# Optimization experiments

Measured on AMD Instinct MI355X. Metric: run time of the kernel, lower is better.

The kernel has to match this reference:

```python
import jax, jax.numpy as jnp
import numpy as np

D_MODEL = 768
STATE_N = 16
BATCH = 8
SEQ = 2048


def setup_inputs() -> dict:
    key = jax.random.key(0)
    ks = jax.random.split(key, 12)
    d, n = D_MODEL, STATE_N
    s = 0.02
    inp = {
        "x": jax.random.normal(ks[0], (BATCH, SEQ, d), dtype=jnp.float32),
        # A_log init as in module: log(arange(1..N)) repeated over d_model
        "A_log": jnp.log(jnp.tile(jnp.arange(1, n + 1, dtype=jnp.float32)[None, :], (d, 1))),
        "D_param": jnp.ones((d,), dtype=jnp.float32),
        "B_proj_w": jax.random.normal(ks[1], (n, d), dtype=jnp.float32) * s,
        "C_proj_w": jax.random.normal(ks[2], (n, d), dtype=jnp.float32) * s,
        "delta_w": jax.random.normal(ks[3], (d, d), dtype=jnp.float32) * s,
        "delta_b": jax.random.normal(ks[4], (d,), dtype=jnp.float32) * s,
        "in_w": jax.random.normal(ks[5], (2 * d, d), dtype=jnp.float32) * s,
        "in_b": jax.random.normal(ks[6], (2 * d,), dtype=jnp.float32) * s,
        "out_w": jax.random.normal(ks[7], (d, d), dtype=jnp.float32) * s,
        "out_b": jax.random.normal(ks[8], (d,), dtype=jnp.float32) * s,
        "conv_w": jax.random.normal(ks[9], (d, 1, 3), dtype=jnp.float32) * s,  # depthwise [D,1,K]
        "conv_b": jax.random.normal(ks[10], (d,), dtype=jnp.float32) * s,
    }
    return inp


def _forward(x, A_log, D_param, B_proj_w, C_proj_w, delta_w, delta_b,
             in_w, in_b, out_w, out_b, conv_w, conv_b):
    A = -jnp.exp(A_log)  # [D, N]
    xz = jnp.einsum("bld,ed->ble", x, in_w) + in_b  # [B, L, 2D]
    x_in, z = jnp.split(xz, 2, axis=-1)
    # depthwise conv1d, padding=1, groups=D (cross-correlation, same as torch)
    x_c = jax.lax.conv_general_dilated(
        jnp.transpose(x_in, (0, 2, 1)), conv_w,
        window_strides=(1,), padding=((1, 1),),
        feature_group_count=x.shape[-1],
        dimension_numbers=("NCH", "OIH", "NCH"))
    x_conv = jnp.transpose(x_c, (0, 2, 1)) + conv_b  # [B, L, D]
    x_conv = jax.nn.silu(x_conv)
    delta = jax.nn.softplus(jnp.einsum("bld,ed->ble", x_conv, delta_w) + delta_b)  # [B,L,D]
    B_sel = jnp.einsum("bld,nd->bln", x_conv, B_proj_w)  # [B, L, N]
    C_sel = jnp.einsum("bld,nd->bln", x_conv, C_proj_w)  # [B, L, N]

    Bsz, L, D = x.shape
    N = A.shape[1]

    def step(h, t_in):
        dt, b_t, c_t, x_t = t_in  # [B,D], [B,N], [B,N], [B,D]
        A_bar = jnp.exp(dt[:, :, None] * A[None, :, :])           # [B,D,N]
        h = A_bar * h + (dt[:, :, None] * b_t[:, None, :]) * x_t[:, :, None]
        y_t = jnp.sum(h * c_t[:, None, :], axis=-1)               # [B,D]
        return h, y_t

    xs = (jnp.transpose(delta, (1, 0, 2)), jnp.transpose(B_sel, (1, 0, 2)),
          jnp.transpose(C_sel, (1, 0, 2)), jnp.transpose(x_conv, (1, 0, 2)))
    h0 = jnp.zeros((Bsz, D, N), dtype=x.dtype)
    _, ys = jax.lax.scan(step, h0, xs)
    y = jnp.transpose(ys, (1, 0, 2))  # [B, L, D]

    y = y + x_conv * D_param[None, None, :]
    y = y * jax.nn.silu(z)
    return jnp.einsum("bld,ed->ble", y, out_w) + out_b


def reference(x, A_log, D_param, B_proj_w, C_proj_w, delta_w, delta_b,
              in_w, in_b, out_w, out_b, conv_w, conv_b):
    return _forward(x, A_log, D_param, B_proj_w, C_proj_w, delta_w, delta_b,
                    in_w, in_b, out_w, out_b, conv_w, conv_b)
```

## Files before the change

### kernel.cpp

```cpp
#include <hip/hip_runtime.h>
#include <hip/hip_bf16.h>

#define D_MODEL 768
#define SEQL    2048
#define BATCH   8
#define NSTATE  16
#define NCHUNK  32
#define TCHUNK  64

typedef __attribute__((ext_vector_type(8))) short short8;
typedef __attribute__((ext_vector_type(4))) float f32x4;

typedef const __attribute__((address_space(1))) unsigned int gas1_t;
typedef __attribute__((address_space(3))) unsigned int las3_t;

__device__ __forceinline__ void gload_lds16(const void* g, void* l) {
  __builtin_amdgcn_global_load_lds((gas1_t*)g, (las3_t*)l, 16, 0, 0);
}

__device__ __forceinline__ float b2f(short s) {
  return __uint_as_float(((unsigned)(unsigned short)s) << 16);
}
__device__ __forceinline__ short f2b(float f) {
  __hip_bfloat16 h = __float2bfloat16(f);
  return *reinterpret_cast<short*>(&h);
}

__global__ __launch_bounds__(256) void prep_all(
    const float* __restrict__ x, const float* __restrict__ in_w,
    const float* __restrict__ delta_w, const float* __restrict__ Bp,
    const float* __restrict__ Cp, const float* __restrict__ out_w,
    const float* __restrict__ A_log,
    __hip_bfloat16* __restrict__ xb, __hip_bfloat16* __restrict__ w_in,
    __hip_bfloat16* __restrict__ w_dbc, __hip_bfloat16* __restrict__ w_out,
    float* __restrict__ A2) {
  int i = blockIdx.x * 256 + threadIdx.x;
  if (i < 3145728) {
    int j = i * 4;
    float4 v = *(const float4*)(x + j);
    xb[j + 0] = __float2bfloat16(v.x);
    xb[j + 1] = __float2bfloat16(v.y);
    xb[j + 2] = __float2bfloat16(v.z);
    xb[j + 3] = __float2bfloat16(v.w);
    return;
  }
  i -= 3145728;
  if (i < 1536 * 768) { w_in[i] = __float2bfloat16(in_w[i]); return; }
  i -= 1536 * 768;
  if (i < 896 * 768) {
    int row = i / 768, col = i - row * 768;
    float v;
    if (row < 768)      v = delta_w[row * 768 + col];
    else if (row < 784) v = Bp[(row - 768) * 768 + col];
    else if (row < 800) v = Cp[(row - 784) * 768 + col];
    else                v = 0.f;
    w_dbc[i] = __float2bfloat16(v);
    return;
  }
  i -= 896 * 768;
  if (i < 768 * 768) { w_out[i] = __float2bfloat16(out_w[i]); return; }
  i -= 768 * 768;
  A2[i] = -expf(A_log[i]) * 1.44269504088896f;
}

template <int MODE>
__global__ __launch_bounds__(256, 3) void gemm128tb(
    const __hip_bfloat16* __restrict__ Amat, const __hip_bfloat16* __restrict__ Bw,
    const float* __restrict__ bias, void* __restrict__ out0,
    void* __restrict__ out1, void* __restrict__ out2, const int gxn) {
  constexpr int K  = 768;
  constexpr int KT = 24;
  __shared__ char lds[49152];
  const int tid  = threadIdx.x;
  const int lane = tid & 63, wave = tid >> 6;
  const int wr = wave >> 1, wc = wave & 1;

  const int nwg = gridDim.x, id = blockIdx.x;
  const int swz = (id & 7) * (nwg >> 3) + (id >> 3);
  const int tm = swz / gxn, tn = swz - tm * gxn;
  const int rowA0 = tm * 128, rowB0 = tn * 128;

  const int srow = tid >> 2;
  const int scol = (((tid & 3) ^ ((srow >> 1) & 3)) << 3);
  const __hip_bfloat16* gA = Amat + (size_t)(rowA0 + srow) * K + scol;
  const __hip_bfloat16* gB = Bw   + (size_t)(rowB0 + srow) * K + scol;
  const int ldst = tid << 4;

  const int frow = lane & 15, fq = lane >> 4;
  const int pc = (fq << 4) ^ (((frow >> 1) & 3) << 4);
  const int aoff = ((wr * 64 + frow) << 6) + pc;
  const int boff = ((wc * 64 + frow) << 6) + pc;

  f32x4 acc[4][4];
#pragma unroll
  for (int m = 0; m < 4; ++m)
#pragma unroll
    for (int n = 0; n < 4; ++n) acc[m][n] = (f32x4){0.f, 0.f, 0.f, 0.f};

#define STAGE(buf, kt)                                                          \
  {                                                                             \
    const __hip_bfloat16* sA = gA + (kt) * 32;                                  \
    const __hip_bfloat16* sB = gB + (kt) * 32;                                  \
    char* dA = lds + (buf) * 16384 + ldst;                                      \
    char* dB = dA + 8192;                                                       \
    gload_lds16(sA, dA);                                                        \
    gload_lds16(sA + (size_t)64 * K, dA + 4096);                                \
    gload_lds16(sB, dB);                                                        \
    gload_lds16(sB + (size_t)64 * K, dB + 4096);                                \
  }
#define VMW(n) asm volatile("s_waitcnt vmcnt(" #n ")" ::: "memory")
#define BAR    __builtin_amdgcn_s_barrier()

  STAGE(0, 0);
  STAGE(1, 1);
  VMW(4);
  BAR;

  int bc = 0;
  for (int kt = 0; kt < KT; ++kt) {
    short8 a[4], b[4];
    const char* ba = lds + bc * 16384;
#pragma unroll
    for (int m = 0; m < 4; ++m) a[m] = *(const short8*)(ba + aoff + m * 1024);
#pragma unroll
    for (int n = 0; n < 4; ++n) b[n] = *(const short8*)(ba + 8192 + boff + n * 1024);
    const bool st = (kt + 2 < KT);
    if (st) {
      const int b2 = bc + 2 >= 3 ? bc - 1 : bc + 2;
      STAGE(b2, kt + 2);
    }
    __builtin_amdgcn_s_setprio(1);
#pragma unroll
    for (int m = 0; m < 4; ++m)
#pragma unroll
      for (int n = 0; n < 4; ++n)
        acc[m][n] = __builtin_amdgcn_mfma_f32_16x16x32_bf16(a[m], b[n], acc[m][n], 0, 0, 0);
    __builtin_amdgcn_s_setprio(0);
    if (st)                VMW(4);
    else if (kt + 2 == KT) VMW(0);
    BAR;
    bc = bc + 1 >= 3 ? 0 : bc + 1;
  }

#pragma unroll
  for (int m = 0; m < 4; ++m) {
    const int grow0 = rowA0 + wr * 64 + m * 16 + fq * 4;
#pragma unroll
    for (int n = 0; n < 4; ++n) {
      const int gcol = rowB0 + wc * 64 + n * 16 + frow;
#pragma unroll
      for (int i = 0; i < 4; ++i) {
        const size_t grow = grow0 + i;
        float v = acc[m][n][i];
        if (MODE == 0) {
          v += bias[gcol];
          if (gcol < 768)
            ((__hip_bfloat16*)out0)[grow * 768 + gcol] = __float2bfloat16(v);
          else
            ((__hip_bfloat16*)out1)[grow * 768 + gcol - 768] = __float2bfloat16(v);
        } else if (MODE == 1) {
          if (gcol < 768) {
            v += bias[gcol];
            float sp = (v > 20.f) ? v : log1pf(expf(v));
            ((__hip_bfloat16*)out0)[grow * 768 + gcol] = __float2bfloat16(sp);
          } else if (gcol < 784) {
            ((float*)out1)[grow * 16 + (gcol - 768)] = v;
          } else if (gcol < 800) {
            ((float*)out2)[grow * 16 + (gcol - 784)] = v;
          }
        } else {
          ((float*)out0)[grow * 768 + gcol] = v + bias[gcol];
        }
      }
    }
  }
#undef STAGE
#undef VMW
#undef BAR
}

__global__ __launch_bounds__(256) void conv_silu8(
    const __hip_bfloat16* __restrict__ xin, const float* __restrict__ conv_w,
    const float* __restrict__ conv_b, __hip_bfloat16* __restrict__ xc) {
  const int idx = blockIdx.x * 256 + threadIdx.x;
  const int d8 = (idx % 96) * 8;
  const int t  = (idx / 96) % SEQL;
  const size_t base = (size_t)idx * 8;

  short8 x0 = *(const short8*)(xin + base);
  short8 xm = {}, xp = {};
  if (t > 0)        xm = *(const short8*)(xin + base - 768);
  if (t < SEQL - 1) xp = *(const short8*)(xin + base + 768);

  const float4* cw4 = (const float4*)(conv_w + d8 * 3);
  float4 cw[6];
#pragma unroll
  for (int q = 0; q < 6; ++q) cw[q] = cw4[q];
  float4 cb0 = *(const float4*)(conv_b + d8);
  float4 cb1 = *(const float4*)(conv_b + d8 + 4);
  const float* cwf = (const float*)cw;
  const float* cbf0 = (const float*)&cb0;
  const float* cbf1 = (const float*)&cb1;

  short8 r;
#pragma unroll
  for (int e = 0; e < 8; ++e) {
    float acc = (e < 4) ? cbf0[e] : cbf1[e - 4];
    acc = fmaf(cwf[e * 3 + 0], b2f(xm[e]), acc);
    acc = fmaf(cwf[e * 3 + 1], b2f(x0[e]), acc);
    acc = fmaf(cwf[e * 3 + 2], b2f(xp[e]), acc);
    const float sig = 1.f / (1.f + __expf(-acc));
    r[e] = f2b(acc * sig);
  }
  *(short8*)(xc + base) = r;
}

__global__ __launch_bounds__(256) void scan_pass1(
    const __hip_bfloat16* __restrict__ delta, const __hip_bfloat16* __restrict__ xconv,
    const float* __restrict__ Bsel, const float* __restrict__ A2,
    float* __restrict__ sumdt, float* __restrict__ Sbuf) {
  const int d = blockIdx.x * 256 + threadIdx.x;
  const int b = blockIdx.y, c = blockIdx.z;
  __shared__ float sB[TCHUNK * 16];
  ((float4*)sB)[threadIdx.x] =
      ((const float4*)(Bsel + ((size_t)b * SEQL + c * TCHUNK) * 16))[threadIdx.x];
  __syncthreads();

  float a2[16];
#pragma unroll
  for (int n = 0; n < 16; ++n) a2[n] = A2[d * 16 + n];
  float h[16] = {};
  float sdt = 0.f;
  const size_t base = ((size_t)b * SEQL + c * TCHUNK) * 768 + d;
  for (int t = 0; t < TCHUNK; ++t) {
    const float dt = b2f(((const short*)delta)[base + (size_t)t * 768]);
    const float x = b2f(((const short*)xconv)[base + (size_t)t * 768]);
    sdt += dt;
    const float dtx = dt * x;
    const float* Br = &sB[t * 16];
#pragma unroll
    for (int n = 0; n < 16; ++n) {
      const float a = exp2f(dt * a2[n]);
      h[n] = fmaf(a, h[n], dtx * Br[n]);
    }
  }
  sumdt[((size_t)b * NCHUNK + c) * 768 + d] = sdt;
#pragma unroll
  for (int n = 0; n < 16; ++n)
    Sbuf[(((size_t)b * NCHUNK + c) * 16 + n) * 768 + d] = h[n];
}

__global__ __launch_bounds__(256) void scan_carry(
    const float* __restrict__ sumdt, const float* __restrict__ Sbuf,
    const float* __restrict__ A2, float* __restrict__ Hin) {
  const int idx = blockIdx.x * 256 + threadIdx.x;
  const int d = idx % 768;
  const int n = (idx / 768) & 15;
  const int b = idx / (768 * 16);
  const float a2 = A2[d * 16 + n];
  float h = 0.f;
  for (int c = 0; c < NCHUNK; ++c) {
    const size_t hb = (((size_t)(b * NCHUNK + c)) * 16 + n) * 768 + d;
    Hin[hb] = h;
    const float sd = sumdt[(b * NCHUNK + c) * 768 + d];
    h = fmaf(exp2f(sd * a2), h, Sbuf[hb]);
  }
}

__global__ __launch_bounds__(256) void scan_pass3(
    const __hip_bfloat16* __restrict__ delta, const __hip_bfloat16* __restrict__ xconv,
    const __hip_bfloat16* __restrict__ zb, const float* __restrict__ Bsel,
    const float* __restrict__ Csel, const float* __restrict__ A2,
    const float* __restrict__ Hin, const float* __restrict__ Dp,
    __hip_bfloat16* __restrict__ yg) {
  const int d = blockIdx.x * 256 + threadIdx.x;
  const int b = blockIdx.y, c = blockIdx.z;
  __shared__ float sB[TCHUNK * 16], sC[TCHUNK * 16];
  {
    const size_t off = ((size_t)b * SEQL + c * TCHUNK) * 16;
    ((float4*)sB)[threadIdx.x] = ((const float4*)(Bsel + off))[threadIdx.x];
    ((float4*)sC)[threadIdx.x] = ((const float4*)(Csel + off))[threadIdx.x];
  }
  __syncthreads();

  float a2[16];
#pragma unroll
  for (int n = 0; n < 16; ++n) a2[n] = A2[d * 16 + n];
  float h[16];
  {
    const size_t hb = ((size_t)b * NCHUNK + c) * 16 * 768 + d;
#pragma unroll
    for (int n = 0; n < 16; ++n) h[n] = Hin[hb + (size_t)n * 768];
  }
  const float Dpd = Dp[d];
  const size_t base = ((size_t)b * SEQL + c * TCHUNK) * 768 + d;
  for (int t = 0; t < TCHUNK; ++t) {
    const float dt = b2f(((const short*)delta)[base + (size_t)t * 768]);
    const float x = b2f(((const short*)xconv)[base + (size_t)t * 768]);
    const float dtx = dt * x;
    const float* Br = &sB[t * 16];
    const float* Cr = &sC[t * 16];
    float y = 0.f;
#pragma unroll
    for (int n = 0; n < 16; ++n) {
      const float a = exp2f(dt * a2[n]);
      h[n] = fmaf(a, h[n], dtx * Br[n]);
      y = fmaf(h[n], Cr[n], y);
    }
    const float z = b2f(((const short*)zb)[base + (size_t)t * 768]);
    const float sig = 1.f / (1.f + __expf(-z));
    const float out = (y + x * Dpd) * (z * sig);
    yg[base + (size_t)t * 768] = __float2bfloat16(out);
  }
}

extern "C" void kernel_launch(void* const* d_in, const int* in_sizes, int n_in,
                              void* d_out, int out_size, void* d_ws, size_t ws_size,
                              hipStream_t stream) {
  const float* x       = (const float*)d_in[0];
  const float* A_log   = (const float*)d_in[1];
  const float* D_param = (const float*)d_in[2];
  const float* B_proj  = (const float*)d_in[3];
  const float* C_proj  = (const float*)d_in[4];
  const float* delta_w = (const float*)d_in[5];
  const float* delta_b = (const float*)d_in[6];
  const float* in_w    = (const float*)d_in[7];
  const float* in_b    = (const float*)d_in[8];
  const float* out_w   = (const float*)d_in[9];
  const float* out_b   = (const float*)d_in[10];
  const float* conv_w  = (const float*)d_in[11];
  const float* conv_b  = (const float*)d_in[12];

  char* ws = (char*)d_ws;
  __hip_bfloat16* xb       = (__hip_bfloat16*)(ws + 0);
  __hip_bfloat16* w_in_b   = (__hip_bfloat16*)(ws + 25165824);
  __hip_bfloat16* w_dbc_b  = (__hip_bfloat16*)(ws + 27525120);
  __hip_bfloat16* w_out_b  = (__hip_bfloat16*)(ws + 28901376);
  float*          A2       = (float*)(ws + 30081024);
  __hip_bfloat16* xin_b    = (__hip_bfloat16*)(ws + 30130176);
  __hip_bfloat16* z_b      = (__hip_bfloat16*)(ws + 55296000);
  __hip_bfloat16* xconv_b  = (__hip_bfloat16*)(ws + 80461824);
  __hip_bfloat16* delta_bf = (__hip_bfloat16*)(ws + 105627648);
  float*          Bsel     = (float*)(ws + 130793472);
  float*          Csel     = (float*)(ws + 131842048);
  float*          sumdt    = (float*)(ws + 132890624);
  float*          Sbuf     = (float*)(ws + 133677056);
  float*          Hin      = (float*)(ws + 146259968);
  __hip_bfloat16* yg       = xb;

  const int BLD = BATCH * SEQL * D_MODEL;

  prep_all<<<21936, 256, 0, stream>>>(x, in_w, delta_w, B_proj, C_proj, out_w, A_log,
                                      xb, w_in_b, w_dbc_b, w_out_b, A2);
  gemm128tb<0><<<1536, 256, 0, stream>>>(xb, w_in_b, in_b, xin_b, z_b, nullptr, 12);
  conv_silu8<<<BLD / 8 / 256, 256, 0, stream>>>(xin_b, conv_w, conv_b, xconv_b);
  gemm128tb<1><<<896, 256, 0, stream>>>(xconv_b, w_dbc_b, delta_b, delta_bf, Bsel, Csel, 7);
  scan_pass1<<<dim3(3, BATCH, NCHUNK), 256, 0, stream>>>(delta_bf, xconv_b, Bsel, A2, sumdt, Sbuf);
  scan_carry<<<384, 256, 0, stream>>>(sumdt, Sbuf, A2, Hin);
  scan_pass3<<<dim3(3, BATCH, NCHUNK), 256, 0, stream>>>(delta_bf, xconv_b, z_b, Bsel, Csel, A2,
                                                         Hin, D_param, yg);
  gemm128tb<2><<<768, 256, 0, stream>>>(yg, w_out_b, out_b, (float*)d_out, nullptr, nullptr, 6);
}
```

Baseline: 347.0 us.

## Store bf16 activations and weights in pre-tiled swizzled layout for contiguous GEMM staging

All bf16 intermediates (x, weights, xin, z, xconv, delta, y) are now written in a 128x32 tile-major layout with the LDS swizzle already applied. The GEMM stages each 8KB k-tile as one contiguous block instead of strided row segments. prep_all also converts 8 elements per thread with packed 16-byte stores. The cost is scattered 2-byte stores in GEMM epilogues and scan kernels whose per-timestep accesses now land in different cache lines. The changed access pattern in the scans could hurt coalescing.

```diff
diff --git a/kernel.cpp b/kernel.cpp
--- a/kernel.cpp
+++ b/kernel.cpp
@@ -26,49 +26,80 @@
   return *reinterpret_cast<short*>(&h);
 }
 
+__device__ __forceinline__ unsigned tix(int r, int k) {
+  return (unsigned)((((r >> 7) * 24 + (k >> 5)) << 13) + ((r & 127) << 6) +
+                    ((((k >> 3) ^ ((r >> 1) & 3)) & 3) << 4) + ((k & 7) << 1));
+}
+
+__device__ __forceinline__ short8 pack8(const float* v) {
+  short8 o;
+#pragma unroll
+  for (int e = 0; e < 8; ++e) o[e] = f2b(v[e]);
+  return o;
+}
+
 __global__ __launch_bounds__(256) void prep_all(
     const float* __restrict__ x, const float* __restrict__ in_w,
     const float* __restrict__ delta_w, const float* __restrict__ Bp,
     const float* __restrict__ Cp, const float* __restrict__ out_w,
     const float* __restrict__ A_log,
-    __hip_bfloat16* __restrict__ xb, __hip_bfloat16* __restrict__ w_in,
-    __hip_bfloat16* __restrict__ w_dbc, __hip_bfloat16* __restrict__ w_out,
+    char* __restrict__ xb, char* __restrict__ w_in,
+    char* __restrict__ w_dbc, char* __restrict__ w_out,
     float* __restrict__ A2) {
   int i = blockIdx.x * 256 + threadIdx.x;
-  if (i < 3145728) {
-    int j = i * 4;
-    float4 v = *(const float4*)(x + j);
-    xb[j + 0] = __float2bfloat16(v.x);
-    xb[j + 1] = __float2bfloat16(v.y);
-    xb[j + 2] = __float2bfloat16(v.z);
-    xb[j + 3] = __float2bfloat16(v.w);
+  if (i < 16384 * 96) {
+    const int r = i / 96, k8 = i - r * 96;
+    float v[8];
+    *(float4*)(v) = *(const float4*)(x + (size_t)r * 768 + k8 * 8);
+    *(float4*)(v + 4) = *(const float4*)(x + (size_t)r * 768 + k8 * 8 + 4);
+    *(short8*)(xb + tix(r, k8 * 8)) = pack8(v);
     return;
   }
-  i -= 3145728;
-  if (i < 1536 * 768) { w_in[i] = __float2bfloat16(in_w[i]); return; }
-  i -= 1536 * 768;
-  if (i < 896 * 768) {
-    int row = i / 768, col = i - row * 768;
-    float v;
-    if (row < 768)      v = delta_w[row * 768 + col];
-    else if (row < 784) v = Bp[(row - 768) * 768 + col];
-    else if (row < 800) v = Cp[(row - 784) * 768 + col];
-    else                v = 0.f;
-    w_dbc[i] = __float2bfloat16(v);
+  i -= 16384 * 96;
+  if (i < 1536 * 96) {
+    const int r = i / 96, k8 = i - r * 96;
+    float v[8];
+    *(float4*)(v) = *(const float4*)(in_w + (size_t)r * 768 + k8 * 8);
+    *(float4*)(v + 4) = *(const float4*)(in_w + (size_t)r * 768 + k8 * 8 + 4);
+    *(short8*)(w_in + tix(r, k8 * 8)) = pack8(v);
     return;
   }
-  i -= 896 * 768;
-  if (i < 768 * 768) { w_out[i] = __float2bfloat16(out_w[i]); return; }
-  i -= 768 * 768;
+  i -= 1536 * 96;
+  if (i < 896 * 96) {
+    const int r = i / 96, k8 = i - r * 96;
+    float v[8];
+    const float* src = (r < 768)   ? delta_w + (size_t)r * 768
+                       : (r < 784) ? Bp + (size_t)(r - 768) * 768
+                       : (r < 800) ? Cp + (size_t)(r - 784) * 768
+                                   : nullptr;
+    if (src) {
+      *(float4*)(v) = *(const float4*)(src + k8 * 8);
+      *(float4*)(v + 4) = *(const float4*)(src + k8 * 8 + 4);
+    } else {
+#pragma unroll
+      for (int e = 0; e < 8; ++e) v[e] = 0.f;
+    }
+    *(short8*)(w_dbc + tix(r, k8 * 8)) = pack8(v);
+    return;
+  }
+  i -= 896 * 96;
+  if (i < 768 * 96) {
+    const int r = i / 96, k8 = i - r * 96;
+    float v[8];
+    *(float4*)(v) = *(const float4*)(out_w + (size_t)r * 768 + k8 * 8);
+    *(float4*)(v + 4) = *(const float4*)(out_w + (size_t)r * 768 + k8 * 8 + 4);
+    *(short8*)(w_out + tix(r, k8 * 8)) = pack8(v);
+    return;
+  }
+  i -= 768 * 96;
   A2[i] = -expf(A_log[i]) * 1.44269504088896f;
 }
 
 template <int MODE>
 __global__ __launch_bounds__(256, 3) void gemm128tb(
-    const __hip_bfloat16* __restrict__ Amat, const __hip_bfloat16* __restrict__ Bw,
+    const char* __restrict__ Amat, const char* __restrict__ Bw,
     const float* __restrict__ bias, void* __restrict__ out0,
     void* __restrict__ out1, void* __restrict__ out2, const int gxn) {
-  constexpr int K  = 768;
   constexpr int KT = 24;
   __shared__ char lds[49152];
   const int tid  = threadIdx.x;
@@ -78,12 +109,9 @@
   const int nwg = gridDim.x, id = blockIdx.x;
   const int swz = (id & 7) * (nwg >> 3) + (id >> 3);
   const int tm = swz / gxn, tn = swz - tm * gxn;
-  const int rowA0 = tm * 128, rowB0 = tn * 128;
-
-  const int srow = tid >> 2;
-  const int scol = (((tid & 3) ^ ((srow >> 1) & 3)) << 3);
-  const __hip_bfloat16* gA = Amat + (size_t)(rowA0 + srow) * K + scol;
-  const __hip_bfloat16* gB = Bw   + (size_t)(rowB0 + srow) * K + scol;
+
+  const char* gA = Amat + ((size_t)tm * KT) * 8192 + (tid << 4);
+  const char* gB = Bw   + ((size_t)tn * KT) * 8192 + (tid << 4);
   const int ldst = tid << 4;
 
   const int frow = lane & 15, fq = lane >> 4;
@@ -99,14 +127,14 @@
 
 #define STAGE(buf, kt)                                                          \
   {                                                                             \
-    const __hip_bfloat16* sA = gA + (kt) * 32;                                  \
-    const __hip_bfloat16* sB = gB + (kt) * 32;                                  \
+    const char* sA = gA + (kt) * 8192;                                          \
+    const char* sB = gB + (kt) * 8192;                                          \
     char* dA = lds + (buf) * 16384 + ldst;                                      \
     char* dB = dA + 8192;                                                       \
     gload_lds16(sA, dA);                                                        \
-    gload_lds16(sA + (size_t)64 * K, dA + 4096);                                \
+    gload_lds16(sA + 4096, dA + 4096);                                          \
     gload_lds16(sB, dB);                                                        \
-    gload_lds16(sB + (size_t)64 * K, dB + 4096);                                \
+    gload_lds16(sB + 4096, dB + 4096);                                          \
   }
 #define VMW(n) asm volatile("s_waitcnt vmcnt(" #n ")" ::: "memory")
 #define BAR    __builtin_amdgcn_s_barrier()
@@ -142,6 +170,7 @@
     bc = bc + 1 >= 3 ? 0 : bc + 1;
   }
 
+  const int rowA0 = tm * 128, rowB0 = tn * 128;
 #pragma unroll
   for (int m = 0; m < 4; ++m) {
     const int grow0 = rowA0 + wr * 64 + m * 16 + fq * 4;
@@ -150,26 +179,26 @@
       const int gcol = rowB0 + wc * 64 + n * 16 + frow;
 #pragma unroll
       for (int i = 0; i < 4; ++i) {
-        const size_t grow = grow0 + i;
+        const int grow = grow0 + i;
         float v = acc[m][n][i];
         if (MODE == 0) {
           v += bias[gcol];
           if (gcol < 768)
-            ((__hip_bfloat16*)out0)[grow * 768 + gcol] = __float2bfloat16(v);
+            *(short*)((char*)out0 + tix(grow, gcol)) = f2b(v);
           else
-            ((__hip_bfloat16*)out1)[grow * 768 + gcol - 768] = __float2bfloat16(v);
+            *(short*)((char*)out1 + tix(grow, gcol - 768)) = f2b(v);
         } else if (MODE == 1) {
           if (gcol < 768) {
             v += bias[gcol];
             float sp = (v > 20.f) ? v : log1pf(expf(v));
-            ((__hip_bfloat16*)out0)[grow * 768 + gcol] = __float2bfloat16(sp);
+            *(short*)((char*)out0 + tix(grow, gcol)) = f2b(sp);
           } else if (gcol < 784) {
-            ((float*)out1)[grow * 16 + (gcol - 768)] = v;
+            ((float*)out1)[(size_t)grow * 16 + (gcol - 768)] = v;
           } else if (gcol < 800) {
-            ((float*)out2)[grow * 16 + (gcol - 784)] = v;
+            ((float*)out2)[(size_t)grow * 16 + (gcol - 784)] = v;
           }
         } else {
-          ((float*)out0)[grow * 768 + gcol] = v + bias[gcol];
+          ((float*)out0)[(size_t)grow * 768 + gcol] = v + bias[gcol];
         }
       }
     }
@@ -180,17 +209,17 @@
 }
 
 __global__ __launch_bounds__(256) void conv_silu8(
-    const __hip_bfloat16* __restrict__ xin, const float* __restrict__ conv_w,
-    const float* __restrict__ conv_b, __hip_bfloat16* __restrict__ xc) {
+    const char* __restrict__ xin, const float* __restrict__ conv_w,
+    const float* __restrict__ conv_b, char* __restrict__ xc) {
   const int idx = blockIdx.x * 256 + threadIdx.x;
-  const int d8 = (idx % 96) * 8;
-  const int t  = (idx / 96) % SEQL;
-  const size_t base = (size_t)idx * 8;
-
-  short8 x0 = *(const short8*)(xin + base);
+  const int r  = idx / 96;
+  const int d8 = (idx - r * 96) * 8;
+  const int t  = r & (SEQL - 1);
+
+  short8 x0 = *(const short8*)(xin + tix(r, d8));
   short8 xm = {}, xp = {};
-  if (t > 0)        xm = *(const short8*)(xin + base - 768);
-  if (t < SEQL - 1) xp = *(const short8*)(xin + base + 768);
+  if (t > 0)        xm = *(const short8*)(xin + tix(r - 1, d8));
+  if (t < SEQL - 1) xp = *(const short8*)(xin + tix(r + 1, d8));
 
   const float4* cw4 = (const float4*)(conv_w + d8 * 3);
   float4 cw[6];
@@ -202,7 +231,7 @@
   const float* cbf0 = (const float*)&cb0;
   const float* cbf1 = (const float*)&cb1;
 
-  short8 r;
+  short8 res;
 #pragma unroll
   for (int e = 0; e < 8; ++e) {
     float acc = (e < 4) ? cbf0[e] : cbf1[e - 4];
@@ -210,13 +239,13 @@
     acc = fmaf(cwf[e * 3 + 1], b2f(x0[e]), acc);
     acc = fmaf(cwf[e * 3 + 2], b2f(xp[e]), acc);
     const float sig = 1.f / (1.f + __expf(-acc));
-    r[e] = f2b(acc * sig);
-  }
-  *(short8*)(xc + base) = r;
+    res[e] = f2b(acc * sig);
+  }
+  *(short8*)(xc + tix(r, d8)) = res;
 }
 
 __global__ __launch_bounds__(256) void scan_pass1(
-    const __hip_bfloat16* __restrict__ delta, const __hip_bfloat16* __restrict__ xconv,
+    const char* __restrict__ delta, const char* __restrict__ xconv,
     const float* __restrict__ Bsel, const float* __restrict__ A2,
     float* __restrict__ sumdt, float* __restrict__ Sbuf) {
   const int d = blockIdx.x * 256 + threadIdx.x;
@@ -231,10 +260,14 @@
   for (int n = 0; n < 16; ++n) a2[n] = A2[d * 16 + n];
   float h[16] = {};
   float sdt = 0.f;
-  const size_t base = ((size_t)b * SEQL + c * TCHUNK) * 768 + d;
+  const int r0 = b * SEQL + c * TCHUNK;
+  const unsigned tb = (((unsigned)((r0 >> 7) * 24 + (d >> 5))) << 13) + ((r0 & 127) << 6);
+  const unsigned sd0 = (d >> 3) & 3;
+  const unsigned klo = (d & 7) << 1;
   for (int t = 0; t < TCHUNK; ++t) {
-    const float dt = b2f(((const short*)delta)[base + (size_t)t * 768]);
-    const float x = b2f(((const short*)xconv)[base + (size_t)t * 768]);
+    const unsigned ro = tb + t * 64 + (((sd0 ^ ((unsigned)t >> 1)) & 3) << 4) + klo;
+    const float dt = b2f(*(const short*)(delta + ro));
+    const float x = b2f(*(const short*)(xconv + ro));
     sdt += dt;
     const float dtx = dt * x;
     const float* Br = &sB[t * 16];
@@ -268,11 +301,11 @@
 }
 
 __global__ __launch_bounds__(256) void scan_pass3(
-    const __hip_bfloat16* __restrict__ delta, const __hip_bfloat16* __restrict__ xconv,
-    const __hip_bfloat16* __restrict__ zb, const float* __restrict__ Bsel,
+    const char* __restrict__ delta, const char* __restrict__ xconv,
+    const char* __restrict__ zb, const float* __restrict__ Bsel,
     const float* __restrict__ Csel, const float* __restrict__ A2,
     const float* __restrict__ Hin, const float* __restrict__ Dp,
-    __hip_bfloat16* __restrict__ yg) {
+    char* __restrict__ yg) {
   const int d = blockIdx.x * 256 + threadIdx.x;
   const int b = blockIdx.y, c = blockIdx.z;
   __shared__ float sB[TCHUNK * 16], sC[TCHUNK * 16];
@@ -293,10 +326,14 @@
     for (int n = 0; n < 16; ++n) h[n] = Hin[hb + (size_t)n * 768];
   }
   const float Dpd = Dp[d];
-  const size_t base = ((size_t)b * SEQL + c * TCHUNK) * 768 + d;
+  const int r0 = b * SEQL + c * TCHUNK;
+  const unsigned tb = (((unsigned)((r0 >> 7) * 24 + (d >> 5))) << 13) + ((r0 & 127) << 6);
+  const unsigned sd0 = (d >> 3) & 3;
+  const unsigned klo = (d & 7) << 1;
   for (int t = 0; t < TCHUNK; ++t) {
-    const float dt = b2f(((const short*)delta)[base + (size_t)t * 768]);
-    const float x = b2f(((const short*)xconv)[base + (size_t)t * 768]);
+    const unsigned ro = tb + t * 64 + (((sd0 ^ ((unsigned)t >> 1)) & 3) << 4) + klo;
+    const float dt = b2f(*(const short*)(delta + ro));
+    const float x = b2f(*(const short*)(xconv + ro));
     const float dtx = dt * x;
     const float* Br = &sB[t * 16];
     const float* Cr = &sC[t * 16];
@@ -307,10 +344,10 @@
       h[n] = fmaf(a, h[n], dtx * Br[n]);
       y = fmaf(h[n], Cr[n], y);
     }
-    const float z = b2f(((const short*)zb)[base + (size_t)t * 768]);
+    const float z = b2f(*(const short*)(zb + ro));
     const float sig = 1.f / (1.f + __expf(-z));
     const float out = (y + x * Dpd) * (z * sig);
-    yg[base + (size_t)t * 768] = __float2bfloat16(out);
+    *(short*)(yg + ro) = f2b(out);
   }
 }
 
@@ -332,28 +369,26 @@
   const float* conv_b  = (const float*)d_in[12];
 
   char* ws = (char*)d_ws;
-  __hip_bfloat16* xb       = (__hip_bfloat16*)(ws + 0);
-  __hip_bfloat16* w_in_b   = (__hip_bfloat16*)(ws + 25165824);
-  __hip_bfloat16* w_dbc_b  = (__hip_bfloat16*)(ws + 27525120);
-  __hip_bfloat16* w_out_b  = (__hip_bfloat16*)(ws + 28901376);
-  float*          A2       = (float*)(ws + 30081024);
-  __hip_bfloat16* xin_b    = (__hip_bfloat16*)(ws + 30130176);
-  __hip_bfloat16* z_b      = (__hip_bfloat16*)(ws + 55296000);
-  __hip_bfloat16* xconv_b  = (__hip_bfloat16*)(ws + 80461824);
-  __hip_bfloat16* delta_bf = (__hip_bfloat16*)(ws + 105627648);
-  float*          Bsel     = (float*)(ws + 130793472);
-  float*          Csel     = (float*)(ws + 131842048);
-  float*          sumdt    = (float*)(ws + 132890624);
-  float*          Sbuf     = (float*)(ws + 133677056);
-  float*          Hin      = (float*)(ws + 146259968);
-  __hip_bfloat16* yg       = xb;
-
-  const int BLD = BATCH * SEQL * D_MODEL;
-
-  prep_all<<<21936, 256, 0, stream>>>(x, in_w, delta_w, B_proj, C_proj, out_w, A_log,
-                                      xb, w_in_b, w_dbc_b, w_out_b, A2);
+  char*  xb       = ws + 0;
+  char*  w_in_b   = ws + 25165824;
+  char*  w_dbc_b  = ws + 27525120;
+  char*  w_out_b  = ws + 28901376;
+  float* A2       = (float*)(ws + 30081024);
+  char*  xin_b    = ws + 30130176;
+  char*  z_b      = ws + 55296000;
+  char*  xconv_b  = ws + 80461824;
+  char*  delta_bf = ws + 105627648;
+  float* Bsel     = (float*)(ws + 130793472);
+  float* Csel     = (float*)(ws + 131842048);
+  float* sumdt    = (float*)(ws + 132890624);
+  float* Sbuf     = (float*)(ws + 133677056);
+  float* Hin      = (float*)(ws + 146259968);
+  char*  yg       = xb;
+
+  prep_all<<<7392, 256, 0, stream>>>(x, in_w, delta_w, B_proj, C_proj, out_w, A_log,
+                                     xb, w_in_b, w_dbc_b, w_out_b, A2);
   gemm128tb<0><<<1536, 256, 0, stream>>>(xb, w_in_b, in_b, xin_b, z_b, nullptr, 12);
-  conv_silu8<<<BLD / 8 / 256, 256, 0, stream>>>(xin_b, conv_w, conv_b, xconv_b);
+  conv_silu8<<<16384 * 96 / 256, 256, 0, stream>>>(xin_b, conv_w, conv_b, xconv_b);
   gemm128tb<1><<<896, 256, 0, stream>>>(xconv_b, w_dbc_b, delta_b, delta_bf, Bsel, Csel, 7);
   scan_pass1<<<dim3(3, BATCH, NCHUNK), 256, 0, stream>>>(delta_bf, xconv_b, Bsel, A2, sumdt, Sbuf);
   scan_carry<<<384, 256, 0, stream>>>(sumdt, Sbuf, A2, Hin);
```

New measurement: 355.6 us. +2.5%, slower.
